# Performance work log

Hardware: AMD Instinct MI355X
Metric: run time of the kernel (lower is better)

## Reference

```python
import jax, jax.numpy as jnp
import numpy as np

B, D = 4096, 512
BASE_TAU = 0.02
CLAMP_MAX = 1e36


def _l2norm(x, eps=1e-12):
    # torch F.normalize(p=2): x / max(||x||, eps)
    n = jnp.sqrt(jnp.sum(x * x, axis=-1, keepdims=True))
    return x / jnp.maximum(n, eps)


def setup_inputs() -> dict:
    key = jax.random.key(0)
    k1, k2, k3, k4, k5, k6 = jax.random.split(key, 6)
    return {
        "visual_feats": jax.random.normal(k1, (B, D), dtype=jnp.float32),
        "textual_feats": jax.random.normal(k2, (B, D), dtype=jnp.float32),
        "pid": jax.random.randint(k3, (B,), 0, 1024, dtype=jnp.int64 if jax.config.jax_enable_x64 else jnp.int32),
        "adaptive_margins": jax.random.uniform(k4, (B,), dtype=jnp.float32),
        "uncertainty_scores": jax.random.uniform(k5, (B,), dtype=jnp.float32),
        "sample_types": jax.random.randint(k6, (B,), 0, 3, dtype=jnp.int64 if jax.config.jax_enable_x64 else jnp.int32),
    }


def reference(visual_feats, textual_feats, pid, adaptive_margins, uncertainty_scores, sample_types):
    tau = BASE_TAU
    vn = _l2norm(visual_feats)
    tn = _l2norm(textual_feats)
    scores = tn @ vn.T  # [B, B]

    # Faithful to the original loop: every iteration i builds a [B,B] matrix
    # whose rows are all scores[i,:] and uses the FULL pid vector, then takes
    # row 0 of the per-sample loss. So the label/mask row is always pid[0]'s.
    labels0 = (pid == pid[0]).astype(scores.dtype)  # [B]
    mask0 = 1.0 - labels0                            # [B]
    n_neg0 = jnp.sum(mask0)

    margins = jax.lax.stop_gradient(adaptive_margins)  # .item() in torch -> no grad

    e = jnp.exp(scores / tau)  # [B, B]
    # i2t branch (row 0 of expanded matrix == scores[i,:], mask row = mask0)
    alpha = jax.lax.stop_gradient(e * labels0 / jnp.sum(e * labels0, axis=1, keepdims=True))  # [B,B]
    neg_sum = jnp.minimum(jnp.sum(e * mask0, axis=1), CLAMP_MAX)  # [B]
    loss_i2t = jnp.maximum(-jnp.sum(alpha * scores, axis=1) + tau * jnp.log(neg_sum) + margins, 0.0)

    # t2i branch: row 0 of expanded.T is scores[i,0] repeated B times;
    # alpha_t2i row 0 sums to 1 so -(alpha*s).sum == -scores[i,0].
    s0 = scores[:, 0]  # [B]
    t2i_sum = jnp.minimum(jnp.exp(s0 / tau) * n_neg0, CLAMP_MAX)
    loss_t2i = jnp.maximum(-s0 + tau * jnp.log(t2i_sum) + margins, 0.0)

    per_sample_losses = loss_i2t + loss_t2i  # [B]

    uncertain = sample_types == 2
    uncertainty_weights = jnp.where(
        uncertain,
        jnp.clip(1.0 - 0.5 * uncertainty_scores, 0.1, 1.0),
        jnp.ones_like(uncertainty_scores),
    )
    final_loss = jnp.sum(per_sample_losses * uncertainty_weights) / jnp.sum(uncertainty_weights)
    return final_loss, per_sample_losses, uncertainty_weights, scores
```

## Files before the change

kernel.cpp:

```cpp
#include <hip/hip_runtime.h>
#include <hip/hip_bf16.h>
#include <stdint.h>

#define NB 4096
#define ND 512
#define TAU_ 0.02f
#define INV_TAU_ 50.0f
#define CLAMP_MAXF 1e36f

typedef __attribute__((ext_vector_type(8))) short bf16x8;
typedef __attribute__((ext_vector_type(4))) float f32x4;

#define AS1(p) ((__attribute__((address_space(1))) void*)(uintptr_t)(p))
#define AS3(p) ((__attribute__((address_space(3))) void*)(uint32_t)(uintptr_t)(p))

static __device__ __forceinline__ unsigned short f2bf(float f) {
  __hip_bfloat16 h = __float2bfloat16(f);
  return *reinterpret_cast<unsigned short*>(&h);
}

__global__ __launch_bounds__(256) void k_norm(const float* __restrict__ vis,
                                              const float* __restrict__ txt,
                                              const int* __restrict__ pid,
                                              unsigned short* __restrict__ tn_b,
                                              unsigned short* __restrict__ vn_b,
                                              float* __restrict__ nneg) {
  if (blockIdx.x == 2048) {
    __shared__ float r4[4];
    int tid = threadIdx.x;
    int pid0 = pid[0];
    float c = 0.f;
    for (int j = tid; j < NB; j += 256) c += (pid[j] != pid0) ? 1.0f : 0.0f;
#pragma unroll
    for (int o = 32; o; o >>= 1) c += __shfl_xor(c, o, 64);
    if ((tid & 63) == 0) r4[tid >> 6] = c;
    __syncthreads();
    if (tid == 0) nneg[0] = r4[0] + r4[1] + r4[2] + r4[3];
    return;
  }
  int wv = threadIdx.x >> 6, ln = threadIdx.x & 63;
  int r = blockIdx.x * 4 + wv;
  const float* src;
  unsigned short* dst;
  if (r < NB) {
    src = txt + (size_t)r * ND;
    dst = tn_b + (size_t)r * ND;
  } else {
    src = vis + (size_t)(r - NB) * ND;
    dst = vn_b + (size_t)(r - NB) * ND;
  }
  float4 x0 = reinterpret_cast<const float4*>(src)[ln];
  float4 x1 = reinterpret_cast<const float4*>(src)[64 + ln];
  float ss = x0.x * x0.x + x0.y * x0.y + x0.z * x0.z + x0.w * x0.w +
             x1.x * x1.x + x1.y * x1.y + x1.z * x1.z + x1.w * x1.w;
#pragma unroll
  for (int o = 32; o; o >>= 1) ss += __shfl_xor(ss, o, 64);
  float inv = 1.0f / fmaxf(sqrtf(ss), 1e-12f);
  ushort4 p0, p1;
  p0.x = f2bf(x0.x * inv); p0.y = f2bf(x0.y * inv);
  p0.z = f2bf(x0.z * inv); p0.w = f2bf(x0.w * inv);
  p1.x = f2bf(x1.x * inv); p1.y = f2bf(x1.y * inv);
  p1.z = f2bf(x1.z * inv); p1.w = f2bf(x1.w * inv);
  reinterpret_cast<ushort4*>(dst)[ln] = p0;
  reinterpret_cast<ushort4*>(dst)[64 + ln] = p1;
}

__global__ __launch_bounds__(512, 2) void k_gemm(const unsigned short* __restrict__ A,
                                                 const unsigned short* __restrict__ Bm,
                                                 const int* __restrict__ pid,
                                                 float* __restrict__ C,
                                                 float* __restrict__ partials,
                                                 float* __restrict__ s0g) {
  __shared__ unsigned short smem[2][2][256 * 64];
  int tid = threadIdx.x;
  int wv = tid >> 6, ln = tid & 63;
  int tile = (blockIdx.x & 7) * 32 + (blockIdx.x >> 3);
  int bm = tile >> 4;
  int bn = tile & 15;
  int wr = wv >> 2, wc = wv & 3;
  int frow = ln & 15, fkg = ln >> 4;
  f32x4 acc[8][4] = {};
  const unsigned short* Abase = A + (size_t)(bm * 256) * ND;
  const unsigned short* Bbase = Bm + (size_t)(bn * 256) * ND;

#define STAGE(buf, k0)                                                          \
  {                                                                             \
    _Pragma("unroll") for (int p = 0; p < 4; ++p) {                             \
      int s = p * 512 + tid;                                                    \
      int rr = s >> 3;                                                          \
      int slot = (s & 7) ^ (rr & 7);            \
      __builtin_amdgcn_global_load_lds(                                         \
          AS1(Abase + (size_t)rr * ND + (k0) + slot * 8),                       \
          AS3((char*)&smem[buf][0][0] + (p * 512 + wv * 64) * 16), 16, 0, 0);   \
      __builtin_amdgcn_global_load_lds(                                         \
          AS1(Bbase + (size_t)rr * ND + (k0) + slot * 8),                       \
          AS3((char*)&smem[buf][1][0] + (p * 512 + wv * 64) * 16), 16, 0, 0);   \
    }                                                                           \
  }

  STAGE(0, 0);
  __syncthreads();
  int buf = 0;
  for (int t = 0; t < 8; ++t) {
    if (t < 7) STAGE(buf ^ 1, (t + 1) * 64);
    const char* pA = (const char*)&smem[buf][0][0];
    const char* pB = (const char*)&smem[buf][1][0];
#pragma unroll
    for (int ksub = 0; ksub < 2; ++ksub) {
      bf16x8 af[8], bfr[4];
#pragma unroll
      for (int mi = 0; mi < 8; ++mi) {
        int row = wr * 128 + mi * 16 + frow;
        af[mi] = *reinterpret_cast<const bf16x8*>(
            pA + row * 128 + (((ksub * 4 + fkg) ^ (row & 7)) * 16));
      }
#pragma unroll
      for (int ni = 0; ni < 4; ++ni) {
        int row = wc * 64 + ni * 16 + frow;
        bfr[ni] = *reinterpret_cast<const bf16x8*>(
            pB + row * 128 + (((ksub * 4 + fkg) ^ (row & 7)) * 16));
      }
#pragma unroll
      for (int mi = 0; mi < 8; ++mi)
#pragma unroll
        for (int ni = 0; ni < 4; ++ni)
          acc[mi][ni] = __builtin_amdgcn_mfma_f32_16x16x32_bf16(af[mi], bfr[ni],
                                                                acc[mi][ni], 0, 0, 0);
    }
    __syncthreads();
    buf ^= 1;
  }

  int pid0 = pid[0];
  int eq[4];
#pragma unroll
  for (int ni = 0; ni < 4; ++ni)
    eq[ni] = (pid[bn * 256 + wc * 64 + ni * 16 + frow] == pid0) ? 1 : 0;
  float* Cp = C + (size_t)(bm * 256 + wr * 128 + fkg * 4) * NB + bn * 256 +
              wc * 64 + frow;
#pragma unroll
  for (int mi = 0; mi < 8; ++mi) {
#pragma unroll
    for (int v = 0; v < 4; ++v) {
      float sp = 0.f, sn = 0.f, sa = 0.f;
      float* rp = Cp + (size_t)(mi * 16 + v) * NB;
#pragma unroll
      for (int ni = 0; ni < 4; ++ni) {
        float s = acc[mi][ni][v];
        rp[ni * 16] = s;
        float e = __expf(s * INV_TAU_);
        if (eq[ni]) {
          sp += e;
          sa += e * s;
        } else {
          sn += e;
        }
      }
#pragma unroll
      for (int o = 1; o < 16; o <<= 1) {
        sp += __shfl_xor(sp, o, 64);
        sn += __shfl_xor(sn, o, 64);
        sa += __shfl_xor(sa, o, 64);
      }
      if (frow == 0) {
        int row = bm * 256 + wr * 128 + mi * 16 + fkg * 4 + v;
        float* po = partials + ((size_t)row * 64 + bn * 4 + wc) * 3;
        po[0] = sp;
        po[1] = sn;
        po[2] = sa;
        if (bn == 0 && wc == 0) s0g[row] = acc[mi][0][v];
      }
    }
  }
}

__global__ __launch_bounds__(256) void k_row2(const float* __restrict__ partials,
                                              const float* __restrict__ s0g,
                                              const float* __restrict__ margins,
                                              const float* __restrict__ unc,
                                              const int* __restrict__ stypes,
                                              const float* __restrict__ nneg,
                                              float* __restrict__ psl,
                                              float* __restrict__ uw) {
  int wv = threadIdx.x >> 6, ln = threadIdx.x & 63;
  int row = blockIdx.x * 4 + wv;
  const float* p = partials + (size_t)row * 64 * 3 + ln * 3;
  float sp = p[0], sn = p[1], sa = p[2];
#pragma unroll
  for (int o = 1; o < 64; o <<= 1) {
    sp += __shfl_xor(sp, o, 64);
    sn += __shfl_xor(sn, o, 64);
    sa += __shfl_xor(sa, o, 64);
  }
  if (ln == 0) {
    float s0v = s0g[row];
    float m = margins[row];
    float li2t = fmaxf(-(sa / sp) + TAU_ * logf(fminf(sn, CLAMP_MAXF)) + m, 0.f);
    float t2i = fminf(__expf(s0v * INV_TAU_) * nneg[0], CLAMP_MAXF);
    float lt2i = fmaxf(-s0v + TAU_ * logf(t2i) + m, 0.f);
    psl[row] = li2t + lt2i;
    float w = 1.f;
    if (stypes[row] == 2) w = fminf(fmaxf(1.f - 0.5f * unc[row], 0.1f), 1.f);
    uw[row] = w;
  }
}

__global__ __launch_bounds__(256) void k_final(const float* __restrict__ psl,
                                               const float* __restrict__ uw,
                                               float* __restrict__ out) {
  __shared__ float rn[4], rd[4];
  int tid = threadIdx.x;
  float num = 0.f, den = 0.f;
  for (int j = tid; j < NB; j += 256) {
    float w = uw[j];
    num += psl[j] * w;
    den += w;
  }
#pragma unroll
  for (int o = 32; o; o >>= 1) {
    num += __shfl_xor(num, o, 64);
    den += __shfl_xor(den, o, 64);
  }
  if ((tid & 63) == 0) {
    rn[tid >> 6] = num;
    rd[tid >> 6] = den;
  }
  __syncthreads();
  if (tid == 0) {
    num = rn[0] + rn[1] + rn[2] + rn[3];
    den = rd[0] + rd[1] + rd[2] + rd[3];
    out[0] = num / den;
  }
}

extern "C" void kernel_launch(void* const* d_in, const int* in_sizes, int n_in,
                              void* d_out, int out_size, void* d_ws, size_t ws_size,
                              hipStream_t stream) {
  const float* vis = (const float*)d_in[0];
  const float* txt = (const float*)d_in[1];
  const int* pid = (const int*)d_in[2];
  const float* margins = (const float*)d_in[3];
  const float* unc = (const float*)d_in[4];
  const int* stypes = (const int*)d_in[5];

  float* out = (float*)d_out;
  float* out_psl = out + 1;
  float* out_uw = out + 1 + NB;
  float* out_scores = out + 1 + 2 * NB;

  unsigned short* tn_b = (unsigned short*)d_ws;
  unsigned short* vn_b = tn_b + (size_t)NB * ND;
  float* nneg = (float*)(vn_b + (size_t)NB * ND);
  float* s0g = nneg + 4;
  float* partials = s0g + NB;

  k_norm<<<2049, 256, 0, stream>>>(vis, txt, pid, tn_b, vn_b, nneg);
  k_gemm<<<256, 512, 0, stream>>>(tn_b, vn_b, pid, out_scores, partials, s0g);
  k_row2<<<NB / 4, 256, 0, stream>>>(partials, s0g, margins, unc, stypes,
                                     nneg, out_psl, out_uw);
  k_final<<<1, 256, 0, stream>>>(out_psl, out_uw, out);
}
```

Measured before the change: 51.59 us.

## Split GEMM block into two independent wave groups with LDS atomic barriers

Restructures the GEMM main loop so each half of the block (4 waves) owns a private 128-row A slab plus its own copy of the B slab. The groups synchronize through LDS atomic counters with spin-waits instead of block-wide __syncthreads. The K step shrinks from 64 to 32 with 16 iterations, and the LDS swizzle changes to a rotation-based scheme. This is meant to remove full-block barrier stalls and let the two groups progress independently. In exchange, B is loaded twice per block, adding global and LDS traffic, and the spin loop with s_sleep adds its own overhead.

```diff
diff --git a/kernel.cpp b/kernel.cpp
--- a/kernel.cpp
+++ b/kernel.cpp
@@ -71,64 +71,78 @@
                                                  float* __restrict__ C,
                                                  float* __restrict__ partials,
                                                  float* __restrict__ s0g) {
-  __shared__ unsigned short smem[2][2][256 * 64];
+  __shared__ unsigned short smem[2][2][384 * 32];
+  __shared__ unsigned int arr[2];
   int tid = threadIdx.x;
   int wv = tid >> 6, ln = tid & 63;
+  int g = wv >> 2, lw = wv & 3;
   int tile = (blockIdx.x & 7) * 32 + (blockIdx.x >> 3);
   int bm = tile >> 4;
   int bn = tile & 15;
-  int wr = wv >> 2, wc = wv & 3;
+  int wc = lw;
   int frow = ln & 15, fkg = ln >> 4;
   f32x4 acc[8][4] = {};
-  const unsigned short* Abase = A + (size_t)(bm * 256) * ND;
+  const unsigned short* Ag = A + (size_t)(bm * 256 + g * 128) * ND;
   const unsigned short* Bbase = Bm + (size_t)(bn * 256) * ND;
-
-#define STAGE(buf, k0)                                                          \
+  if (tid < 2) arr[tid] = 0;
+  __syncthreads();
+
+#define STAGE_G(bufi, k0)                                                       \
   {                                                                             \
-    _Pragma("unroll") for (int p = 0; p < 4; ++p) {                             \
-      int s = p * 512 + tid;                                                    \
-      int rr = s >> 3;                                                          \
-      int slot = (s & 7) ^ (rr & 7);            \
+    char* lb = (char*)&smem[g][bufi][0];                                        \
+    _Pragma("unroll") for (int p = 0; p < 2; ++p) {                             \
+      int s = p * 256 + lw * 64 + ln;                                           \
+      int rr = s >> 2;                                                          \
+      int sg = ((s & 3) + (rr >> 1)) & 3;                                       \
       __builtin_amdgcn_global_load_lds(                                         \
-          AS1(Abase + (size_t)rr * ND + (k0) + slot * 8),                       \
-          AS3((char*)&smem[buf][0][0] + (p * 512 + wv * 64) * 16), 16, 0, 0);   \
+          AS1(Ag + (size_t)rr * ND + (k0) + sg * 8),                            \
+          AS3(lb + (p * 256 + lw * 64) * 16), 16, 0, 0);                        \
+    }                                                                           \
+    _Pragma("unroll") for (int p = 2; p < 6; ++p) {                             \
+      int s = p * 256 + lw * 64 + ln;                                           \
+      int rr = s >> 2;                                                          \
+      int sg = ((s & 3) + (rr >> 1)) & 3;                                       \
       __builtin_amdgcn_global_load_lds(                                         \
-          AS1(Bbase + (size_t)rr * ND + (k0) + slot * 8),                       \
-          AS3((char*)&smem[buf][1][0] + (p * 512 + wv * 64) * 16), 16, 0, 0);   \
+          AS1(Bbase + (size_t)(rr - 128) * ND + (k0) + sg * 8),                 \
+          AS3(lb + (p * 256 + lw * 64) * 16), 16, 0, 0);                        \
     }                                                                           \
   }
 
-  STAGE(0, 0);
-  __syncthreads();
-  int buf = 0;
-  for (int t = 0; t < 8; ++t) {
-    if (t < 7) STAGE(buf ^ 1, (t + 1) * 64);
-    const char* pA = (const char*)&smem[buf][0][0];
-    const char* pB = (const char*)&smem[buf][1][0];
-#pragma unroll
-    for (int ksub = 0; ksub < 2; ++ksub) {
-      bf16x8 af[8], bfr[4];
-#pragma unroll
-      for (int mi = 0; mi < 8; ++mi) {
-        int row = wr * 128 + mi * 16 + frow;
-        af[mi] = *reinterpret_cast<const bf16x8*>(
-            pA + row * 128 + (((ksub * 4 + fkg) ^ (row & 7)) * 16));
-      }
-#pragma unroll
-      for (int ni = 0; ni < 4; ++ni) {
-        int row = wc * 64 + ni * 16 + frow;
-        bfr[ni] = *reinterpret_cast<const bf16x8*>(
-            pB + row * 128 + (((ksub * 4 + fkg) ^ (row & 7)) * 16));
-      }
-#pragma unroll
-      for (int mi = 0; mi < 8; ++mi)
-#pragma unroll
-        for (int ni = 0; ni < 4; ++ni)
-          acc[mi][ni] = __builtin_amdgcn_mfma_f32_16x16x32_bf16(af[mi], bfr[ni],
-                                                                acc[mi][ni], 0, 0, 0);
+  STAGE_G(0, 0);
+  for (int t = 0; t < 16; ++t) {
+    asm volatile("s_waitcnt vmcnt(0)" ::: "memory");
+    if (ln == 0)
+      __hip_atomic_fetch_add(&arr[g], 1u, __ATOMIC_RELEASE,
+                             __HIP_MEMORY_SCOPE_WORKGROUP);
+    unsigned need = (unsigned)(4 * (t + 1));
+    while (__hip_atomic_load(&arr[g], __ATOMIC_ACQUIRE,
+                             __HIP_MEMORY_SCOPE_WORKGROUP) < need)
+      __builtin_amdgcn_s_sleep(1);
+    __builtin_amdgcn_sched_barrier(0);
+    if (t < 15) STAGE_G((t + 1) & 1, (t + 1) * 32);
+    const char* pA = (const char*)&smem[g][t & 1][0];
+    const char* pB = pA + 128 * 64;
+    bf16x8 af[8], bfr[4];
+#pragma unroll
+    for (int ni = 0; ni < 4; ++ni) {
+      int rb = wc * 64 + ni * 16 + frow;
+      bfr[ni] = *reinterpret_cast<const bf16x8*>(
+          pB + rb * 64 + (((fkg - (rb >> 1)) & 3) * 16));
     }
-    __syncthreads();
-    buf ^= 1;
+#pragma unroll
+    for (int mi = 0; mi < 8; ++mi) {
+      int r = mi * 16 + frow;
+      af[mi] = *reinterpret_cast<const bf16x8*>(
+          pA + r * 64 + (((fkg - (r >> 1)) & 3) * 16));
+    }
+#pragma unroll
+    for (int mi = 0; mi < 8; ++mi)
+#pragma unroll
+      for (int ni = 0; ni < 4; ++ni)
+        acc[mi][ni] = __builtin_amdgcn_mfma_f32_16x16x32_bf16(af[mi], bfr[ni],
+                                                              acc[mi][ni], 0, 0, 0);
+    asm volatile("s_waitcnt lgkmcnt(0)" ::: "memory");
+    __builtin_amdgcn_sched_barrier(0);
   }
 
   int pid0 = pid[0];
@@ -136,7 +150,7 @@
 #pragma unroll
   for (int ni = 0; ni < 4; ++ni)
     eq[ni] = (pid[bn * 256 + wc * 64 + ni * 16 + frow] == pid0) ? 1 : 0;
-  float* Cp = C + (size_t)(bm * 256 + wr * 128 + fkg * 4) * NB + bn * 256 +
+  float* Cp = C + (size_t)(bm * 256 + g * 128 + fkg * 4) * NB + bn * 256 +
               wc * 64 + frow;
 #pragma unroll
   for (int mi = 0; mi < 8; ++mi) {
@@ -163,7 +177,7 @@
         sa += __shfl_xor(sa, o, 64);
       }
       if (frow == 0) {
-        int row = bm * 256 + wr * 128 + mi * 16 + fkg * 4 + v;
+        int row = bm * 256 + g * 128 + mi * 16 + fkg * 4 + v;
         float* po = partials + ((size_t)row * 64 + bn * 4 + wc) * 3;
         po[0] = sp;
         po[1] = sn;
```

New measurement: 53.92 us. 1.05x slower.
